# Optimization experiments

Hardware: AMD Instinct MI355X
Metric: run time of the kernel (lower is better)

## Reference

```python
import jax, jax.numpy as jnp
import numpy as np

N_U, N_I, D, RANK, NNZ = 100000, 50000, 64, 64, 1000000
L, TEMP, LAMBDA_1, DROPOUT, BATCH_USER, EPS = 2, 0.2, 0.2, 0.1, 2048, 0.05
B = 2048


def _leaky(x):
    return jnp.where(x >= 0, x, 0.5 * x)


def _l2norm(x):
    n = jnp.sqrt(jnp.sum(x * x, axis=1, keepdims=True))
    return x / jnp.maximum(n, 1e-12)


def setup_inputs() -> dict:
    key = jax.random.key(0)
    ks = jax.random.split(key, 24)
    xav = 0.05
    inp = {
        'E_u_0': jax.random.normal(ks[0], (N_U, D), jnp.float32) * xav,
        'E_i_0': jax.random.normal(ks[1], (N_I, D), jnp.float32) * xav,
        'svd_u': jax.random.normal(ks[2], (N_U, RANK), jnp.float32) * xav,
        'svd_v': jax.random.normal(ks[3], (N_I, RANK), jnp.float32) * xav,
        's': jax.random.uniform(ks[4], (RANK,), jnp.float32),
        'ut': jax.random.normal(ks[5], (RANK, N_U), jnp.float32) * xav,
        'vt': jax.random.normal(ks[6], (RANK, N_I), jnp.float32) * xav,
        'W_u': jax.random.normal(ks[7], (L, D, D), jnp.float32) * xav,
        'W_i': jax.random.normal(ks[8], (L, D, D), jnp.float32) * xav,
        'adj_vals': jax.random.uniform(ks[9], (NNZ,), jnp.float32),
        'drop_rand': jax.random.uniform(ks[10], (L, 2, NNZ), jnp.float32),
        'noise_u1': jax.random.uniform(ks[11], (N_U, RANK), jnp.float32),
        'noise_v1': jax.random.uniform(ks[12], (N_I, RANK), jnp.float32),
        'noise_u2': jax.random.uniform(ks[13], (N_U, RANK), jnp.float32),
        'noise_v2': jax.random.uniform(ks[14], (N_I, RANK), jnp.float32),
        'u_mask_raw': jax.random.uniform(ks[15], (L, B), jnp.float32),
        'i_mask_raw': jax.random.uniform(ks[16], (L, B), jnp.float32),
        'adj_rows': jax.random.randint(ks[17], (NNZ,), 0, N_U, jnp.int32),
        'adj_cols': jax.random.randint(ks[18], (NNZ,), 0, N_I, jnp.int32),
        'uids': jax.random.randint(ks[19], (B,), 0, N_U, jnp.int32),
        'iids': jax.random.randint(ks[20], (B,), 0, N_I, jnp.int32),
        'pos': jax.random.randint(ks[21], (B,), 0, N_I, jnp.int32),
        'neg': jax.random.randint(ks[22], (B,), 0, N_I, jnp.int32),
    }
    return inp


def _forward(E_u_0, E_i_0, svd_u, svd_v, s, ut, vt, W_u, W_i, adj_vals,
             drop_rand, noise_u1, noise_v1, noise_u2, noise_v2,
             u_mask_raw, i_mask_raw, adj_rows, adj_cols, uids, iids, pos, neg):
    # --- SVD low-rank augmentation with sign-aligned uniform noise ---
    def perturb(svd, noise):
        return svd + jnp.sign(svd) * _l2norm(noise) * EPS

    svd_u_1, svd_v_1 = perturb(svd_u, noise_u1), perturb(svd_v, noise_v1)
    svd_u_2, svd_v_2 = perturb(svd_u, noise_u2), perturb(svd_v, noise_v2)
    u_mul_s_1 = svd_u_1 * s  # [n_u, r] @ diag(s)
    v_mul_s_1 = svd_v_1 * s
    u_mul_s_2 = svd_u_2 * s
    v_mul_s_2 = svd_v_2 * s

    def spmm_drop(vals_mask_rand, E, seg_ids, gather_ids, n_out):
        keep = (vals_mask_rand >= DROPOUT).astype(adj_vals.dtype)
        dv = adj_vals * keep / (1.0 - DROPOUT)  # sparse dropout w/ rescale
        msgs = dv[:, None] * E[gather_ids]       # [nnz, d]
        return jax.ops.segment_sum(msgs, seg_ids, num_segments=n_out)

    E_u_list, E_i_list = [E_u_0], [E_i_0]
    G_u_1, G_i_1, G_u_2, G_i_2 = [None], [None], [None], [None]
    for layer in range(1, L + 1):
        Eu_p, Ei_p = E_u_list[layer - 1], E_i_list[layer - 1]
        Z_u = _leaky(spmm_drop(drop_rand[layer - 1, 0], Ei_p, adj_rows, adj_cols, N_U))
        Z_i = _leaky(spmm_drop(drop_rand[layer - 1, 1], Eu_p, adj_cols, adj_rows, N_I))
        vt_ei = vt @ Ei_p   # [r, d]
        ut_eu = ut @ Eu_p   # [r, d]
        G_u_1.append(_leaky(u_mul_s_1 @ vt_ei))
        G_i_1.append(_leaky(v_mul_s_1 @ ut_eu))
        G_u_2.append(_leaky(u_mul_s_2 @ vt_ei))
        G_i_2.append(_leaky(v_mul_s_2 @ ut_eu))
        E_u_list.append(Z_u + Eu_p)
        E_i_list.append(Z_i + Ei_p)

    E_u = sum(E_u_list)
    E_i = sum(E_i_list)

    # --- contrastive InfoNCE between the two augmented views ---
    def cl_loss(g1, g2, ids, W, mask_raw):
        mask = (mask_raw > 0.5).astype(g1.dtype)
        h1 = _l2norm(g1[ids]) @ W
        h2 = _l2norm(g2[ids]) @ W
        pos_score = jnp.exp(jnp.sum(h1 * h2, axis=1) / TEMP)
        neg_score = jnp.sum(jnp.exp(h1 @ h2.T / TEMP), axis=1)
        return jnp.sum(-jnp.log(pos_score / (neg_score + 1e-8) + 1e-8) * mask)

    loss_s = jnp.asarray(0.0, E_u.dtype)
    for lyr in range(1, L + 1):
        loss_s = loss_s + cl_loss(G_u_1[lyr], G_u_2[lyr], uids, W_u[lyr - 1], u_mask_raw[lyr - 1])
        loss_s = loss_s + cl_loss(G_i_1[lyr], G_i_2[lyr], iids, W_i[lyr - 1], i_mask_raw[lyr - 1])

    # --- BPR-style hinge loss (vectorized over the batch loop) ---
    u_emb = E_u[uids]
    pos_sc = jnp.sum(u_emb * E_i[pos], axis=1)
    neg_sc = jnp.sum(u_emb * E_i[neg], axis=1)
    loss_r = jnp.sum(jax.nn.relu(1.0 - pos_sc + neg_sc)) / BATCH_USER

    loss = loss_r + LAMBDA_1 * loss_s
    return (loss, loss_r, loss_s)


def reference(E_u_0, E_i_0, svd_u, svd_v, s, ut, vt, W_u, W_i, adj_vals,
              drop_rand, noise_u1, noise_v1, noise_u2, noise_v2,
              u_mask_raw, i_mask_raw, adj_rows, adj_cols, uids, iids, pos, neg):
    return _forward(E_u_0, E_i_0, svd_u, svd_v, s, ut, vt, W_u, W_i, adj_vals,
                    drop_rand, noise_u1, noise_v1, noise_u2, noise_v2,
                    u_mask_raw, i_mask_raw, adj_rows, adj_cols, uids, iids, pos, neg)
```

## Files before the change

kernel.cpp:

```cpp
#include <hip/hip_runtime.h>
#include <cstddef>

#define N_U   100000
#define N_I   50000
#define DD    64
#define NNZ_  1000000
#define LL    2
#define TEMP_ 0.2f
#define LAM1  0.2f
#define DROP_ 0.1f
#define EPS_  0.05f
#define BB    2048
#define KCH   320
#define NCH_I ((N_I + KCH - 1) / KCH)
#define NCH_U ((N_U + KCH - 1) / KCH)
#define REGION_SZ 2097152

__device__ __forceinline__ float leaky(float x) { return x >= 0.0f ? x : 0.5f * x; }

__device__ __forceinline__ float waveReduceSum(float v) {
#pragma unroll
  for (int m = 32; m >= 1; m >>= 1) v += __shfl_xor(v, m, 64);
  return v;
}

__device__ __forceinline__ int rlanei(int v, int l) {
  return __builtin_amdgcn_readlane(v, l);
}
__device__ __forceinline__ float rlanef(float v, int l) {
  return __int_as_float(__builtin_amdgcn_readlane(__float_as_int(v), l));
}

__device__ __forceinline__ void gload_lds16(const float* g, float* l) {
  __builtin_amdgcn_global_load_lds(
      (const __attribute__((address_space(1))) void*)g,
      (__attribute__((address_space(3))) void*)l, 16, 0, 0);
}

__global__ void hist_kernel(const int* __restrict__ rows, const int* __restrict__ cols,
                            int* __restrict__ deg_u, int* __restrict__ deg_i, int nnz) {
  int e = blockIdx.x * blockDim.x + threadIdx.x;
  if (e >= nnz) return;
  atomicAdd(&deg_u[rows[e]], 1);
  atomicAdd(&deg_i[cols[e]], 1);
}

__global__ void scan1(const int* __restrict__ in, int* __restrict__ tmp,
                      int* __restrict__ partial, int n) {
  __shared__ int s[256];
  int t = threadIdx.x;
  int base = blockIdx.x * 1024;
  int v[4]; int tsum = 0;
#pragma unroll
  for (int k = 0; k < 4; ++k) {
    int idx = base + t * 4 + k;
    v[k] = (idx < n) ? in[idx] : 0;
    tsum += v[k];
  }
  s[t] = tsum;
  __syncthreads();
  for (int ofs = 1; ofs < 256; ofs <<= 1) {
    int x = (t >= ofs) ? s[t - ofs] : 0;
    __syncthreads();
    s[t] += x;
    __syncthreads();
  }
  if (t == 255) partial[blockIdx.x] = s[255];
  int run = (t == 0) ? 0 : s[t - 1];
#pragma unroll
  for (int k = 0; k < 4; ++k) {
    run += v[k];
    int idx = base + t * 4 + k;
    if (idx < n) tmp[idx] = run;
  }
}

__global__ void scan2(int* __restrict__ partial, int nb) {
  __shared__ int s[256];
  int t = threadIdx.x;
  s[t] = (t < nb) ? partial[t] : 0;
  __syncthreads();
  for (int ofs = 1; ofs < 256; ofs <<= 1) {
    int x = (t >= ofs) ? s[t - ofs] : 0;
    __syncthreads();
    s[t] += x;
    __syncthreads();
  }
  if (t < nb) partial[t] = (t == 0) ? 0 : s[t - 1];
}

__global__ void scan3(const int* __restrict__ tmp, const int* __restrict__ partial,
                      int* __restrict__ off, int n) {
  int i = blockIdx.x * blockDim.x + threadIdx.x;
  if (i == 0) off[0] = 0;
  if (i < n) off[i + 1] = tmp[i] + partial[i >> 10];
}

__global__ void scatter_build(const int* __restrict__ rows, const int* __restrict__ cols,
                              const float* __restrict__ vals, const float* __restrict__ dropr,
                              const int* __restrict__ off_u, const int* __restrict__ off_i,
                              int* __restrict__ cur_u, int* __restrict__ cur_i,
                              float4* __restrict__ pu, float4* __restrict__ pi,
                              int nnz) {
  int e = blockIdx.x * blockDim.x + threadIdx.x;
  if (e >= nnz) return;
  int r = rows[e], c = cols[e];
  float v = vals[e] * (1.0f / (1.0f - DROP_));
  float k0 = (dropr[e] >= DROP_) ? v : 0.0f;
  float k1 = (dropr[(size_t)NNZ_ + e] >= DROP_) ? v : 0.0f;
  float k2 = (dropr[(size_t)2 * NNZ_ + e] >= DROP_) ? v : 0.0f;
  float k3 = (dropr[(size_t)3 * NNZ_ + e] >= DROP_) ? v : 0.0f;
  int p = off_u[r] + atomicAdd(&cur_u[r], 1);
  pu[p] = make_float4(__int_as_float(c), k0, k2, 0.0f);
  int q = off_i[c] + atomicAdd(&cur_i[c], 1);
  pi[q] = make_float4(__int_as_float(r), k1, k3, 0.0f);
}

__global__ void spmm_all(const int* __restrict__ off_u, const float4* __restrict__ pu,
                         const int* __restrict__ off_i, const float4* __restrict__ pi,
                         const float* __restrict__ Eu0, const float* __restrict__ Ei0,
                         float* __restrict__ EU1, float* __restrict__ EI1) {
  int wid = threadIdx.x >> 6, lane = threadIdx.x & 63;
  int r = blockIdx.x * 4 + wid;
  const int* off; const float4* pay;
  const float* Esrc; const float* base; float* out;
  if (r < N_U) {
    off = off_u; pay = pu; Esrc = Ei0; base = Eu0; out = EU1;
  } else {
    r -= N_U;
    if (r >= N_I) return;
    off = off_i; pay = pi; Esrc = Eu0; base = Ei0; out = EI1;
  }
  int i0 = off[r], i1 = off[r + 1];
  float acc = 0.0f;
  for (int p = i0; p < i1; p += 64) {
    int cn = min(64, i1 - p);
    float dvl = 0.0f; int gl = 0;
    if (lane < cn) {
      float4 pl = pay[p + lane];
      gl = __float_as_int(pl.x);
      dvl = pl.y;
    }
    int j = 0;
    for (; j + 3 < cn; j += 4) {
      float d0 = rlanef(dvl, j), d1 = rlanef(dvl, j + 1),
            d2 = rlanef(dvl, j + 2), d3 = rlanef(dvl, j + 3);
      int g0 = rlanei(gl, j), g1 = rlanei(gl, j + 1),
          g2 = rlanei(gl, j + 2), g3 = rlanei(gl, j + 3);
      float e0 = Esrc[(size_t)g0 * DD + lane];
      float e1 = Esrc[(size_t)g1 * DD + lane];
      float e2 = Esrc[(size_t)g2 * DD + lane];
      float e3 = Esrc[(size_t)g3 * DD + lane];
      acc += d0 * e0; acc += d1 * e1; acc += d2 * e2; acc += d3 * e3;
    }
    for (; j < cn; ++j)
      acc += rlanef(dvl, j) * Esrc[(size_t)rlanei(gl, j) * DD + lane];
  }
  size_t o = (size_t)r * DD + lane;
  out[o] = base[o] + leaky(acc);
}

__global__ void spmm_batch3(const int* __restrict__ uids, const int* __restrict__ pos,
                            const int* __restrict__ neg,
                            const int* __restrict__ off_u, const float4* __restrict__ pu,
                            const int* __restrict__ off_i, const float4* __restrict__ pi,
                            const float* __restrict__ EU1, const float* __restrict__ EI1,
                            float* __restrict__ bu, float* __restrict__ bpos,
                            float* __restrict__ bneg) {
  int z = blockIdx.y;
  const int* ids = (z == 0) ? uids : ((z == 1) ? pos : neg);
  const int* off = (z == 0) ? off_u : off_i;
  const float4* pay = (z == 0) ? pu : pi;
  const float* Esrc = (z == 0) ? EI1 : EU1;
  const float* base = (z == 0) ? EU1 : EI1;
  float* out = (z == 0) ? bu : ((z == 1) ? bpos : bneg);
  int wid = threadIdx.x >> 6, lane = threadIdx.x & 63;
  int i = blockIdx.x * 4 + wid;
  int r = ids[i];
  int i0 = off[r], i1 = off[r + 1];
  float acc = 0.0f;
  for (int p = i0; p < i1; p += 64) {
    int cn = min(64, i1 - p);
    float dvl = 0.0f; int gl = 0;
    if (lane < cn) {
      float4 pl = pay[p + lane];
      gl = __float_as_int(pl.x);
      dvl = pl.z;
    }
    int j = 0;
    for (; j + 3 < cn; j += 4) {
      float d0 = rlanef(dvl, j), d1 = rlanef(dvl, j + 1),
            d2 = rlanef(dvl, j + 2), d3 = rlanef(dvl, j + 3);
      int g0 = rlanei(gl, j), g1 = rlanei(gl, j + 1),
          g2 = rlanei(gl, j + 2), g3 = rlanei(gl, j + 3);
      acc += d0 * Esrc[(size_t)g0 * DD + lane];
      acc += d1 * Esrc[(size_t)g1 * DD + lane];
      acc += d2 * Esrc[(size_t)g2 * DD + lane];
      acc += d3 * Esrc[(size_t)g3 * DD + lane];
    }
    for (; j < cn; ++j)
      acc += rlanef(dvl, j) * Esrc[(size_t)rlanei(gl, j) * DD + lane];
  }
  out[(size_t)i * DD + lane] = base[(size_t)r * DD + lane] + leaky(acc);
}

__global__ void gemm_tiled(const float* __restrict__ A0, const float* __restrict__ B0,
                           const float* __restrict__ A1, const float* __restrict__ B1,
                           float* __restrict__ Cp) {
  __shared__ __align__(16) float sA[2][4096];
  __shared__ __align__(16) float sB[2][4096];
  int bx = blockIdx.x;
  const float* A; const float* B; int N; int k0;
  if (bx < NCH_I) { A = A0; B = B0; N = N_I; k0 = bx * KCH; }
  else            { A = A1; B = B1; N = N_U; k0 = (bx - NCH_I) * KCH; }
  int t = threadIdx.x;
  int w = t >> 6, l = t & 63;
  int rseg = l >> 4;
  int c4 = (l & 15) * 4;
  int ti = t >> 4, tj = t & 15;
  int ti4 = ti * 4, tj4 = tj * 4;

  int NT = min(KCH / 64, (N - k0 + 63) >> 6);

  float acc[4][4];
#pragma unroll
  for (int x = 0; x < 4; ++x)
#pragma unroll
    for (int y = 0; y < 4; ++y) acc[x][y] = 0.0f;

  auto stage = [&](int tt, int b) {
    int kb = k0 + tt * 64;
    if (kb + 64 <= N) {
#pragma unroll
      for (int q = 0; q < 4; ++q) {
        int s = w * 4 + q;
        const float* ga = A + (size_t)(s * 4 + rseg) * N + kb + c4;
        gload_lds16(ga, &sA[b][s * 256]);
        const float* gb = B + (size_t)(kb + s * 4 + rseg) * DD + c4;
        gload_lds16(gb, &sB[b][s * 256]);
      }
    } else {
#pragma unroll
      for (int q = 0; q < 16; ++q) {
        int lin = t + q * 256;
        int r = lin >> 6, c = lin & 63;
        sA[b][lin] = (kb + c < N) ? A[(size_t)r * N + kb + c] : 0.0f;
        sB[b][lin] = (kb + r < N) ? B[(size_t)(kb + r) * DD + c] : 0.0f;
      }
    }
  };

  stage(0, 0);
  __syncthreads();
  int cur = 0;
  for (int tt = 0; tt < NT; ++tt) {
    if (tt + 1 < NT) stage(tt + 1, cur ^ 1);
    const float* cA = sA[cur];
    const float* cB = sB[cur];
#pragma unroll 8
    for (int k = 0; k < 64; ++k) {
      float4 b4 = *(const float4*)&cB[k * 64 + tj4];
      float a0 = cA[(ti4 + 0) * 64 + k];
      float a1 = cA[(ti4 + 1) * 64 + k];
      float a2 = cA[(ti4 + 2) * 64 + k];
      float a3 = cA[(ti4 + 3) * 64 + k];
      acc[0][0] += a0 * b4.x; acc[0][1] += a0 * b4.y; acc[0][2] += a0 * b4.z; acc[0][3] += a0 * b4.w;
      acc[1][0] += a1 * b4.x; acc[1][1] += a1 * b4.y; acc[1][2] += a1 * b4.z; acc[1][3] += a1 * b4.w;
      acc[2][0] += a2 * b4.x; acc[2][1] += a2 * b4.y; acc[2][2] += a2 * b4.z; acc[2][3] += a2 * b4.w;
      acc[3][0] += a3 * b4.x; acc[3][1] += a3 * b4.y; acc[3][2] += a3 * b4.z; acc[3][3] += a3 * b4.w;
    }
    __syncthreads();
    cur ^= 1;
  }

  float* cp = Cp + (size_t)bx * 4096;
#pragma unroll
  for (int x = 0; x < 4; ++x)
#pragma unroll
    for (int y = 0; y < 4; ++y)
      cp[(ti4 + x) * DD + tj4 + y] = acc[x][y];
}

__global__ void gemm_reduce_s1(const float* __restrict__ Cp, float* __restrict__ Cp2) {
  int y = blockIdx.y, z = blockIdx.z;
  const float* base = Cp + (y ? (size_t)NCH_I * 4096 : 0);
  int cnt = y ? NCH_U : NCH_I;
  int chunk = (cnt + 3) >> 2;
  int b0 = z * chunk, b1 = min(b0 + chunk, cnt);
  int idx = blockIdx.x * 256 + threadIdx.x;
  float s = 0.0f;
  for (int b = b0; b < b1; ++b) s += base[(size_t)b * 4096 + idx];
  Cp2[((size_t)(y * 4 + z)) * 4096 + idx] = s;
}

__global__ void gemm_reduce_s2(const float* __restrict__ Cp2,
                               float* __restrict__ C0, float* __restrict__ C1) {
  int y = blockIdx.y;
  float* C = y ? C1 : C0;
  int idx = blockIdx.x * 256 + threadIdx.x;
  float s = 0.0f;
#pragma unroll
  for (int z = 0; z < 4; ++z) s += Cp2[((size_t)(y * 4 + z)) * 4096 + idx];
  C[idx] = s;
}

__global__ void h_kernel2(const float* __restrict__ svd,
                          const float* __restrict__ n1, const float* __restrict__ n2,
                          const float* __restrict__ sdiag,
                          const float* __restrict__ Mb,
                          const float* __restrict__ Wb,
                          const int*   __restrict__ ids,
                          float*       __restrict__ hout) {
  int layer = blockIdx.y;
  const float* M = Mb + layer * 4096;
  const float* W = Wb + layer * 4096;
  int wid  = threadIdx.x >> 6;
  int lane = threadIdx.x & 63;
  int i = blockIdx.x * 4 + wid;
  int id = ids[i];
  float sv = svd[(size_t)id * DD + lane];
  float sgn = (sv > 0.0f) ? 1.0f : ((sv < 0.0f) ? -1.0f : 0.0f);
  float sd = sdiag[lane];

  float z1 = n1[(size_t)id * DD + lane];
  float z2 = n2[(size_t)id * DD + lane];
  float d1 = fmaxf(sqrtf(waveReduceSum(z1 * z1)), 1e-12f);
  float d2 = fmaxf(sqrtf(waveReduceSum(z2 * z2)), 1e-12f);
  float g1 = (sv + sgn * (z1 / d1) * EPS_) * sd;
  float g2 = (sv + sgn * (z2 / d2) * EPS_) * sd;

  float a1 = 0.0f, a2 = 0.0f;
#pragma unroll
  for (int k = 0; k < 64; ++k) {
    float m = M[k * DD + lane];
    a1 += rlanef(g1, k) * m;
    a2 += rlanef(g2, k) * m;
  }
  a1 = leaky(a1); a2 = leaky(a2);
  float s1 = fmaxf(sqrtf(waveReduceSum(a1 * a1)), 1e-12f);
  float s2 = fmaxf(sqrtf(waveReduceSum(a2 * a2)), 1e-12f);
  float gn1 = a1 / s1, gn2 = a2 / s2;

  float h1 = 0.0f, h2 = 0.0f;
#pragma unroll
  for (int k = 0; k < 64; ++k) {
    float w = W[k * DD + lane];
    h1 += rlanef(gn1, k) * w;
    h2 += rlanef(gn2, k) * w;
  }
  size_t b0 = ((size_t)(layer * 2 + 0) * BB + i) * DD + lane;
  size_t b1 = ((size_t)(layer * 2 + 1) * BB + i) * DD + lane;
  hout[b0] = h1;
  hout[b1] = h2;
}

__global__ void score_tiles(const float* __restrict__ hu, const float* __restrict__ hv,
                            float* __restrict__ negpart) {
  __shared__ float s1[64][65];
  __shared__ float s2[64][65];
  int z = blockIdx.z;
  int layer = z >> 1, side = z & 1;
  const float* hb = side ? hv : hu;
  const float* h1 = hb + (size_t)(layer * 2 + 0) * BB * DD;
  const float* h2 = hb + (size_t)(layer * 2 + 1) * BB * DD;
  int i0 = blockIdx.x * 64, j0 = blockIdx.y * 64;
  int t = threadIdx.x;
#pragma unroll
  for (int k = 0; k < 16; ++k) {
    int lin = t + k * 256;
    int r = lin >> 6, c = lin & 63;
    s1[r][c] = h1[(size_t)(i0 + r) * DD + c];
    s2[r][c] = h2[(size_t)(j0 + r) * DD + c];
  }
  __syncthreads();
  int ti = t >> 4, tj = t & 15;
  float acc[4][4];
#pragma unroll
  for (int x = 0; x < 4; ++x)
#pragma unroll
    for (int y = 0; y < 4; ++y) acc[x][y] = 0.0f;
  for (int d = 0; d < 64; ++d) {
    float a[4], b[4];
#pragma unroll
    for (int k = 0; k < 4; ++k) { a[k] = s1[ti * 4 + k][d]; b[k] = s2[tj * 4 + k][d]; }
#pragma unroll
    for (int x = 0; x < 4; ++x)
#pragma unroll
      for (int y = 0; y < 4; ++y) acc[x][y] += a[x] * b[y];
  }
  float rsum[4];
#pragma unroll
  for (int x = 0; x < 4; ++x) {
    float s = 0.0f;
#pragma unroll
    for (int y = 0; y < 4; ++y) s += expf(acc[x][y] * (1.0f / TEMP_));
    rsum[x] = s;
  }
  __syncthreads();
#pragma unroll
  for (int x = 0; x < 4; ++x) s1[ti * 4 + x][tj] = rsum[x];
  __syncthreads();
  if (t < 64) {
    float s = 0.0f;
#pragma unroll
    for (int c = 0; c < 16; ++c) s += s1[t][c];
    negpart[((size_t)z * 32 + blockIdx.y) * BB + i0 + t] = s;
  }
}

__global__ void score_loss(const float* __restrict__ hu, const float* __restrict__ hv,
                           const float* __restrict__ negpart,
                           const float* __restrict__ u_mask, const float* __restrict__ i_mask,
                           float* __restrict__ loss_acc) {
  __shared__ float red[256];
  int z = blockIdx.y;
  int layer = z >> 1, side = z & 1;
  const float* hb = side ? hv : hu;
  const float* h1 = hb + (size_t)(layer * 2 + 0) * BB * DD;
  const float* h2 = hb + (size_t)(layer * 2 + 1) * BB * DD;
  const float* mask = (side ? i_mask : u_mask) + layer * BB;
  int i = blockIdx.x * 256 + threadIdx.x;
  const float4* a = (const float4*)(h1 + (size_t)i * DD);
  const float4* b = (const float4*)(h2 + (size_t)i * DD);
  float pos = 0.0f;
#pragma unroll
  for (int k = 0; k < 16; ++k) {
    float4 av = a[k], bv = b[k];
    pos += av.x * bv.x + av.y * bv.y + av.z * bv.z + av.w * bv.w;
  }
  float ng = 0.0f;
  for (int jt = 0; jt < 32; ++jt) ng += negpart[((size_t)z * 32 + jt) * BB + i];
  float ps = expf(pos * (1.0f / TEMP_));
  float m = (mask[i] > 0.5f) ? 1.0f : 0.0f;
  float li = -logf(ps / (ng + 1e-8f) + 1e-8f) * m;
  red[threadIdx.x] = li;
  __syncthreads();
  for (int ofs = 128; ofs >= 1; ofs >>= 1) {
    if (threadIdx.x < ofs) red[threadIdx.x] += red[threadIdx.x + ofs];
    __syncthreads();
  }
  if (threadIdx.x == 0) unsafeAtomicAdd(loss_acc, red[0]);
}

__global__ void bpr_kernel(const float* __restrict__ Eu0, const float* __restrict__ EU1,
                           const float* __restrict__ bu,
                           const float* __restrict__ Ei0, const float* __restrict__ EI1,
                           const float* __restrict__ bpos, const float* __restrict__ bneg,
                           const int* __restrict__ uids, const int* __restrict__ pos,
                           const int* __restrict__ neg,
                           float* __restrict__ acc_r) {
  __shared__ float red[256];
  int i = blockIdx.x * 256 + threadIdx.x;
  const float4* u0 = (const float4*)(Eu0 + (size_t)uids[i] * DD);
  const float4* u1 = (const float4*)(EU1 + (size_t)uids[i] * DD);
  const float4* u2 = (const float4*)(bu  + (size_t)i * DD);
  const float4* p0 = (const float4*)(Ei0 + (size_t)pos[i] * DD);
  const float4* p1 = (const float4*)(EI1 + (size_t)pos[i] * DD);
  const float4* p2 = (const float4*)(bpos + (size_t)i * DD);
  const float4* n0 = (const float4*)(Ei0 + (size_t)neg[i] * DD);
  const float4* n1 = (const float4*)(EI1 + (size_t)neg[i] * DD);
  const float4* n2 = (const float4*)(bneg + (size_t)i * DD);
  float ps = 0.0f, ns = 0.0f;
#pragma unroll
  for (int k = 0; k < 16; ++k) {
    float4 ua = u0[k], ub = u1[k], uc = u2[k];
    float4 pa = p0[k], pb = p1[k], pc = p2[k];
    float4 na = n0[k], nb = n1[k], nc = n2[k];
    float ux = ua.x + ub.x + uc.x, uy = ua.y + ub.y + uc.y,
          uz = ua.z + ub.z + uc.z, uw = ua.w + ub.w + uc.w;
    ps += ux * (pa.x + pb.x + pc.x) + uy * (pa.y + pb.y + pc.y)
        + uz * (pa.z + pb.z + pc.z) + uw * (pa.w + pb.w + pc.w);
    ns += ux * (na.x + nb.x + nc.x) + uy * (na.y + nb.y + nc.y)
        + uz * (na.z + nb.z + nc.z) + uw * (na.w + nb.w + nc.w);
  }
  red[threadIdx.x] = fmaxf(1.0f - ps + ns, 0.0f);
  __syncthreads();
  for (int ofs = 128; ofs >= 1; ofs >>= 1) {
    if (threadIdx.x < ofs) red[threadIdx.x] += red[threadIdx.x + ofs];
    __syncthreads();
  }
  if (threadIdx.x == 0) unsafeAtomicAdd(acc_r, red[0]);
}

__global__ void finalize_kernel(const float* __restrict__ acc, float* __restrict__ out) {
  float lr = acc[0] / (float)BB;
  float ls = acc[1];
  out[0] = lr + LAM1 * ls;
  out[1] = lr;
  out[2] = ls;
}

extern "C" void kernel_launch(void* const* d_in, const int* in_sizes, int n_in,
                              void* d_out, int out_size, void* d_ws, size_t ws_size,
                              hipStream_t stream) {
  const float* E_u_0   = (const float*)d_in[0];
  const float* E_i_0   = (const float*)d_in[1];
  const float* svd_u   = (const float*)d_in[2];
  const float* svd_v   = (const float*)d_in[3];
  const float* sdiag   = (const float*)d_in[4];
  const float* ut      = (const float*)d_in[5];
  const float* vt      = (const float*)d_in[6];
  const float* W_u     = (const float*)d_in[7];
  const float* W_i     = (const float*)d_in[8];
  const float* adjv    = (const float*)d_in[9];
  const float* dropr   = (const float*)d_in[10];
  const float* noise_u1= (const float*)d_in[11];
  const float* noise_v1= (const float*)d_in[12];
  const float* noise_u2= (const float*)d_in[13];
  const float* noise_v2= (const float*)d_in[14];
  const float* u_mask  = (const float*)d_in[15];
  const float* i_mask  = (const float*)d_in[16];
  const int*   rows    = (const int*)d_in[17];
  const int*   cols    = (const int*)d_in[18];
  const int*   uids    = (const int*)d_in[19];
  const int*   iids    = (const int*)d_in[20];
  const int*   pos     = (const int*)d_in[21];
  const int*   neg     = (const int*)d_in[22];
  float* out = (float*)d_out;

  float* ws     = (float*)d_ws;
  float* EU1    = ws;
  float* EI1    = EU1 + (size_t)N_U * DD;
  float* vtei   = EI1 + (size_t)N_I * DD;
  float* uteu   = vtei + 2 * DD * DD;
  float* accs   = uteu + 2 * DD * DD;
  float* region = accs + 16;
  float* Cp   = region;
  float* Cp2  = Cp + (size_t)(NCH_I + NCH_U) * 4096;
  float* bu   = region;
  float* bpos = bu   + (size_t)BB * DD;
  float* bneg = bpos + (size_t)BB * DD;
  float* hu   = bneg + (size_t)BB * DD;
  float* hv   = hu   + (size_t)4 * BB * DD;
  float* negp = hv   + (size_t)4 * BB * DD;
  float4* pu  = (float4*)(region + (size_t)REGION_SZ);
  float4* pi  = pu + NNZ_;
  int* off_u = (int*)(pi + NNZ_);
  int* off_i = off_u + (N_U + 1);
  int* cur_u = off_i + (N_I + 1);
  int* cur_i = cur_u + N_U;
  int* spart = cur_i + N_I;
  int* stmp  = (int*)pu;
  int* deg_u = (int*)pi;
  int* deg_i = deg_u + N_U;

  const int TB = 256;
  dim3 blk(TB);
  int eg = (NNZ_ + TB - 1) / TB;
  int row_grid = BB / 4;

  hipMemsetAsync(deg_u, 0, (size_t)(N_U + N_I) * sizeof(int), stream);
  hipMemsetAsync(cur_u, 0, (size_t)(N_U + N_I) * sizeof(int), stream);
  hipMemsetAsync(accs, 0, 16 * sizeof(float), stream);

  hist_kernel<<<eg, blk, 0, stream>>>(rows, cols, deg_u, deg_i, NNZ_);
  {
    int nb_u = (N_U + 1023) / 1024, nb_i = (N_I + 1023) / 1024;
    scan1<<<nb_u, blk, 0, stream>>>(deg_u, stmp, spart, N_U);
    scan2<<<1, blk, 0, stream>>>(spart, nb_u);
    scan3<<<(N_U + TB - 1) / TB, blk, 0, stream>>>(stmp, spart, off_u, N_U);
    scan1<<<nb_i, blk, 0, stream>>>(deg_i, stmp, spart, N_I);
    scan2<<<1, blk, 0, stream>>>(spart, nb_i);
    scan3<<<(N_I + TB - 1) / TB, blk, 0, stream>>>(stmp, spart, off_i, N_I);
  }
  scatter_build<<<eg, blk, 0, stream>>>(rows, cols, adjv, dropr, off_u, off_i,
                                        cur_u, cur_i, pu, pi, NNZ_);

  gemm_tiled<<<NCH_I + NCH_U, blk, 0, stream>>>(vt, E_i_0, ut, E_u_0, Cp);
  gemm_reduce_s1<<<dim3(16, 2, 4), blk, 0, stream>>>(Cp, Cp2);
  gemm_reduce_s2<<<dim3(16, 2), blk, 0, stream>>>(Cp2, vtei, uteu);

  spmm_all<<<(N_U + N_I + 3) / 4, blk, 0, stream>>>(off_u, pu, off_i, pi,
                                                    E_u_0, E_i_0, EU1, EI1);

  gemm_tiled<<<NCH_I + NCH_U, blk, 0, stream>>>(vt, EI1, ut, EU1, Cp);
  gemm_reduce_s1<<<dim3(16, 2, 4), blk, 0, stream>>>(Cp, Cp2);
  gemm_reduce_s2<<<dim3(16, 2), blk, 0, stream>>>(Cp2, vtei + 4096, uteu + 4096);

  spmm_batch3<<<dim3(row_grid, 3), blk, 0, stream>>>(uids, pos, neg,
      off_u, pu, off_i, pi, EU1, EI1, bu, bpos, bneg);

  h_kernel2<<<dim3(row_grid, LL), blk, 0, stream>>>(svd_u, noise_u1, noise_u2, sdiag,
                                                    vtei, W_u, uids, hu);
  h_kernel2<<<dim3(row_grid, LL), blk, 0, stream>>>(svd_v, noise_v1, noise_v2, sdiag,
                                                    uteu, W_i, iids, hv);
  score_tiles<<<dim3(32, 32, 4), blk, 0, stream>>>(hu, hv, negp);
  score_loss<<<dim3(8, 4), blk, 0, stream>>>(hu, hv, negp, u_mask, i_mask, accs + 1);

  bpr_kernel<<<8, blk, 0, stream>>>(E_u_0, EU1, bu, E_i_0, EI1, bpos, bneg,
                                    uids, pos, neg, accs);

  finalize_kernel<<<1, 1, 0, stream>>>(accs, out);
}
```

Measured before the change: 729.9 us.

## Build CSR via two-pass bucketed binning and merge user/item scan kernels

Replaces the single random-scatter CSR construction with a two-pass scheme. Each block bins its edges by coarse row bucket in shared memory and writes contiguous slabs to a staging buffer. A second pass then places records into their final rows while working within a bucket, so the final writes stay within localized address ranges. The user and item prefix scans are merged into single launches using blockIdx.y, which cuts the number of launches. The cost is extra launches for the binning passes, a staging buffer in the workspace, and an extra read/write of the full payload.

```diff
diff --git a/kernel.cpp b/kernel.cpp
--- a/kernel.cpp
+++ b/kernel.cpp
@@ -16,6 +16,13 @@
 #define NCH_U ((N_U + KCH - 1) / KCH)
 #define REGION_SZ 2097152
 
+#define NBK   196
+#define SH_U  9
+#define SH_I  8
+#define C1_CHUNK   3072
+#define C1_THREADS 512
+#define C1_EPT     6
+
 __device__ __forceinline__ float leaky(float x) { return x >= 0.0f ? x : 0.5f * x; }
 
 __device__ __forceinline__ float waveReduceSum(float v) {
@@ -45,8 +52,15 @@
   atomicAdd(&deg_i[cols[e]], 1);
 }
 
-__global__ void scan1(const int* __restrict__ in, int* __restrict__ tmp,
-                      int* __restrict__ partial, int n) {
+__global__ void scan1b(const int* __restrict__ deg_u, const int* __restrict__ deg_i,
+                       int* __restrict__ tmp_u, int* __restrict__ tmp_i,
+                       int* __restrict__ part_u, int* __restrict__ part_i) {
+  int y = blockIdx.y;
+  const int* in = y ? deg_i : deg_u;
+  int n = y ? N_I : N_U;
+  int* tmp = y ? tmp_i : tmp_u;
+  int* partial = y ? part_i : part_u;
+  if (blockIdx.x * 1024 >= n) return;
   __shared__ int s[256];
   int t = threadIdx.x;
   int base = blockIdx.x * 1024;
@@ -75,7 +89,10 @@
   }
 }
 
-__global__ void scan2(int* __restrict__ partial, int nb) {
+__global__ void scan2b(int* __restrict__ part_u, int* __restrict__ part_i) {
+  int y = blockIdx.y;
+  int* partial = y ? part_i : part_u;
+  int nb = y ? (N_I + 1023) / 1024 : (N_U + 1023) / 1024;
   __shared__ int s[256];
   int t = threadIdx.x;
   s[t] = (t < nb) ? partial[t] : 0;
@@ -89,31 +106,104 @@
   if (t < nb) partial[t] = (t == 0) ? 0 : s[t - 1];
 }
 
-__global__ void scan3(const int* __restrict__ tmp, const int* __restrict__ partial,
-                      int* __restrict__ off, int n) {
+__global__ void scan3b(const int* __restrict__ tmp_u, const int* __restrict__ tmp_i,
+                       const int* __restrict__ part_u, const int* __restrict__ part_i,
+                       int* __restrict__ off_u, int* __restrict__ off_i) {
+  int y = blockIdx.y;
+  const int* tmp = y ? tmp_i : tmp_u;
+  const int* partial = y ? part_i : part_u;
+  int* off = y ? off_i : off_u;
+  int n = y ? N_I : N_U;
   int i = blockIdx.x * blockDim.x + threadIdx.x;
   if (i == 0) off[0] = 0;
   if (i < n) off[i + 1] = tmp[i] + partial[i >> 10];
 }
 
-__global__ void scatter_build(const int* __restrict__ rows, const int* __restrict__ cols,
-                              const float* __restrict__ vals, const float* __restrict__ dropr,
-                              const int* __restrict__ off_u, const int* __restrict__ off_i,
-                              int* __restrict__ cur_u, int* __restrict__ cur_i,
-                              float4* __restrict__ pu, float4* __restrict__ pi,
-                              int nnz) {
-  int e = blockIdx.x * blockDim.x + threadIdx.x;
-  if (e >= nnz) return;
-  int r = rows[e], c = cols[e];
-  float v = vals[e] * (1.0f / (1.0f - DROP_));
-  float k0 = (dropr[e] >= DROP_) ? v : 0.0f;
-  float k1 = (dropr[(size_t)NNZ_ + e] >= DROP_) ? v : 0.0f;
-  float k2 = (dropr[(size_t)2 * NNZ_ + e] >= DROP_) ? v : 0.0f;
-  float k3 = (dropr[(size_t)3 * NNZ_ + e] >= DROP_) ? v : 0.0f;
-  int p = off_u[r] + atomicAdd(&cur_u[r], 1);
-  pu[p] = make_float4(__int_as_float(c), k0, k2, 0.0f);
-  int q = off_i[c] + atomicAdd(&cur_i[c], 1);
-  pi[q] = make_float4(__int_as_float(r), k1, k3, 0.0f);
+__global__ __launch_bounds__(C1_THREADS)
+void csr_bin(const int* __restrict__ rws,
+             const int* __restrict__ oth,
+             const float* __restrict__ vals,
+             const float* __restrict__ dA, const float* __restrict__ dB,
+             const int* __restrict__ off,
+             int* __restrict__ bcur,
+             float4* __restrict__ stg,
+             int shift) {
+  __shared__ float4 st[C1_CHUNK];
+  __shared__ int hist[NBK], lbase[NBK], cur2[NBK], slab[NBK], lboff[NBK];
+  __shared__ int sc[256];
+  int t = threadIdx.x;
+  int e0 = blockIdx.x * C1_CHUNK;
+  int n = min(C1_CHUNK, NNZ_ - e0);
+  for (int b = t; b < NBK; b += C1_THREADS) { hist[b] = 0; cur2[b] = 0; }
+  __syncthreads();
+  int myr[C1_EPT], myo[C1_EPT];
+  float mk1[C1_EPT], mk2[C1_EPT];
+#pragma unroll
+  for (int k = 0; k < C1_EPT; ++k) {
+    int li = t + k * C1_THREADS;
+    if (li < n) {
+      int e = e0 + li;
+      int r = rws[e];
+      myr[k] = r;
+      myo[k] = oth[e];
+      float v = vals[e] * (1.0f / (1.0f - DROP_));
+      mk1[k] = (dA[e] >= DROP_) ? v : 0.0f;
+      mk2[k] = (dB[e] >= DROP_) ? v : 0.0f;
+      atomicAdd(&hist[r >> shift], 1);
+    } else {
+      myr[k] = -1;
+    }
+  }
+  __syncthreads();
+  if (t < 256) sc[t] = (t < NBK) ? hist[t] : 0;
+  __syncthreads();
+  for (int ofs = 1; ofs < 256; ofs <<= 1) {
+    int x = (t < 256 && t >= ofs) ? sc[t - ofs] : 0;
+    __syncthreads();
+    if (t < 256) sc[t] += x;
+    __syncthreads();
+  }
+  if (t < NBK) {
+    lbase[t] = (t == 0) ? 0 : sc[t - 1];
+    lboff[t] = off[t << shift];
+    if (hist[t] > 0) slab[t] = atomicAdd(&bcur[t], hist[t]);
+  }
+  __syncthreads();
+#pragma unroll
+  for (int k = 0; k < C1_EPT; ++k) {
+    if (myr[k] >= 0) {
+      int b = myr[k] >> shift;
+      int pos = lbase[b] + atomicAdd(&cur2[b], 1);
+      st[pos] = make_float4(__int_as_float(myo[k]), mk1[k], mk2[k],
+                            __int_as_float(myr[k]));
+    }
+  }
+  __syncthreads();
+  for (int s = t; s < n; s += C1_THREADS) {
+    float4 rec = st[s];
+    int r = __float_as_int(rec.w);
+    int b = r >> shift;
+    stg[(size_t)lboff[b] + slab[b] + (s - lbase[b])] = rec;
+  }
+}
+
+__global__ void csr_place(const float4* __restrict__ stg, const int* __restrict__ off,
+                          int* __restrict__ cur, float4* __restrict__ out,
+                          int N, int shift) {
+  int b = blockIdx.x;
+  int lo = off[b << shift];
+  int hiRow = (b + 1) << shift; if (hiRow > N) hiRow = N;
+  int hi = off[hiRow];
+  int cnt = hi - lo;
+  int part = blockIdx.y;
+  int c0 = lo + (int)(((long long)cnt * part) >> 2);
+  int c1 = lo + (int)(((long long)cnt * (part + 1)) >> 2);
+  for (int i = c0 + threadIdx.x; i < c1; i += blockDim.x) {
+    float4 rec = stg[i];
+    int r = __float_as_int(rec.w);
+    int pos = off[r] + atomicAdd(&cur[r], 1);
+    out[pos] = rec;
+  }
 }
 
 __global__ void spmm_all(const int* __restrict__ off_u, const float4* __restrict__ pu,
@@ -539,8 +629,14 @@
   int* off_i = off_u + (N_U + 1);
   int* cur_u = off_i + (N_I + 1);
   int* cur_i = cur_u + N_U;
-  int* spart = cur_i + N_I;
-  int* stmp  = (int*)pu;
+  int* bcur_u = cur_i + N_I;
+  int* bcur_i = bcur_u + NBK;
+  int* spart_u = bcur_i + NBK;
+  int* spart_i = spart_u + 256;
+  float4* stg_u = (float4*)ws;
+  float4* stg_i = stg_u + NNZ_;
+  int* stmp_u = (int*)pu;
+  int* stmp_i = stmp_u + N_U;
   int* deg_u = (int*)pi;
   int* deg_i = deg_u + N_U;
 
@@ -550,21 +646,28 @@
   int row_grid = BB / 4;
 
   hipMemsetAsync(deg_u, 0, (size_t)(N_U + N_I) * sizeof(int), stream);
-  hipMemsetAsync(cur_u, 0, (size_t)(N_U + N_I) * sizeof(int), stream);
+  hipMemsetAsync(cur_u, 0, (size_t)(N_U + N_I + 2 * NBK) * sizeof(int), stream);
   hipMemsetAsync(accs, 0, 16 * sizeof(float), stream);
 
   hist_kernel<<<eg, blk, 0, stream>>>(rows, cols, deg_u, deg_i, NNZ_);
   {
-    int nb_u = (N_U + 1023) / 1024, nb_i = (N_I + 1023) / 1024;
-    scan1<<<nb_u, blk, 0, stream>>>(deg_u, stmp, spart, N_U);
-    scan2<<<1, blk, 0, stream>>>(spart, nb_u);
-    scan3<<<(N_U + TB - 1) / TB, blk, 0, stream>>>(stmp, spart, off_u, N_U);
-    scan1<<<nb_i, blk, 0, stream>>>(deg_i, stmp, spart, N_I);
-    scan2<<<1, blk, 0, stream>>>(spart, nb_i);
-    scan3<<<(N_I + TB - 1) / TB, blk, 0, stream>>>(stmp, spart, off_i, N_I);
-  }
-  scatter_build<<<eg, blk, 0, stream>>>(rows, cols, adjv, dropr, off_u, off_i,
-                                        cur_u, cur_i, pu, pi, NNZ_);
+    int nb_u = (N_U + 1023) / 1024;
+    scan1b<<<dim3(nb_u, 2), blk, 0, stream>>>(deg_u, deg_i, stmp_u, stmp_i,
+                                              spart_u, spart_i);
+    scan2b<<<dim3(1, 2), blk, 0, stream>>>(spart_u, spart_i);
+    scan3b<<<dim3((N_U + TB - 1) / TB, 2), blk, 0, stream>>>(stmp_u, stmp_i,
+                                                             spart_u, spart_i,
+                                                             off_u, off_i);
+  }
+  {
+    int c1g = (NNZ_ + C1_CHUNK - 1) / C1_CHUNK;
+    csr_bin<<<c1g, C1_THREADS, 0, stream>>>(rows, cols, adjv,
+        dropr, dropr + (size_t)2 * NNZ_, off_u, bcur_u, stg_u, SH_U);
+    csr_bin<<<c1g, C1_THREADS, 0, stream>>>(cols, rows, adjv,
+        dropr + (size_t)NNZ_, dropr + (size_t)3 * NNZ_, off_i, bcur_i, stg_i, SH_I);
+    csr_place<<<dim3(NBK, 4), blk, 0, stream>>>(stg_u, off_u, cur_u, pu, N_U, SH_U);
+    csr_place<<<dim3(NBK, 4), blk, 0, stream>>>(stg_i, off_i, cur_i, pi, N_I, SH_I);
+  }
 
   gemm_tiled<<<NCH_I + NCH_U, blk, 0, stream>>>(vt, E_i_0, ut, E_u_0, Cp);
   gemm_reduce_s1<<<dim3(16, 2, 4), blk, 0, stream>>>(Cp, Cp2);
```

After: 706.9 us. -3.1%, faster.
